# Kernel optimization log

Hardware: AMD Instinct MI355X
Metric: run time of the kernel (lower is better)

Reference implementation:

```python
import jax, jax.numpy as jnp
import numpy as np

IN_F, OUT_F = 64, 32
N = IN_F * OUT_F + OUT_F  # 2080 sampled parameters (weights + bias)
B, S = 8, 2048
SCALE_INIT = 1.0 * float(np.sqrt(2.0 / (IN_F + OUT_F)))


def setup_inputs() -> dict:
    key = jax.random.key(0)
    k_x, k_eps, k_loc, k_cov = jax.random.split(key, 4)
    x = jax.random.normal(k_x, (B, S, IN_F), dtype=jnp.float32)
    eps = jax.random.normal(k_eps, (B, S, N), dtype=jnp.float32)
    loc = 0.01 * jax.random.normal(k_loc, (N,), dtype=jnp.float32)
    logvar = jnp.full((N,), float(np.log(SCALE_INIT)), dtype=jnp.float32)
    n_off = N * (N - 1) // 2
    cov_flat = 0.001 * jax.random.normal(k_cov, (n_off,), dtype=jnp.float32)
    return {"x": x, "eps": eps, "loc": loc, "logvar": logvar, "cov_flat": cov_flat}


def reference(x, eps, loc, logvar, cov_flat):
    n = loc.shape[0]
    in_f = x.shape[-1]
    out_f = n // (in_f + 1)  # n = out*(in+1)
    # flat_to_triangular (strictly lower) + make_cholesky, vectorized scatter
    rows, cols = np.tril_indices(n, -1)
    A = jnp.zeros((n, n), dtype=x.dtype).at[rows, cols].set(cov_flat)
    L = A + jnp.diag(jnp.exp(logvar * 0.5))  # off-diag from cov, diag = std
    # MultivariateNormal rsample: loc + L @ eps (per batch sample)
    W = loc + jnp.einsum('bsn,mn->bsm', eps, L)  # [B,S,N]
    b = W[..., :out_f]
    Wm = W[..., out_f:].reshape(*W.shape[:-1], in_f, out_f)  # [B,S,in,out]
    y = jnp.einsum('bsh,bshk->bsk', x, Wm) + b
    return y
```

## Files before the change

### kernel.cpp

```cpp
#include <hip/hip_runtime.h>
#include <hip/hip_bf16.h>

#define IN_F  64
#define OUT_F 32
#define NV    2080
#define NPAD  2176
#define MM    16384
#define KK    2080
#define NBN   17
#define BM    256

typedef __attribute__((ext_vector_type(4))) float f32x4;
typedef __bf16 bf16x8 __attribute__((ext_vector_type(8)));

using gas_ptr = const __attribute__((address_space(1))) void*;
using lds_ptr = __attribute__((address_space(3))) void*;

__global__ __launch_bounds__(256) void build_L_k(const float* __restrict__ cov,
                                                 const float* __restrict__ logvar,
                                                 __hip_bfloat16* __restrict__ LB) {
    const int idx = blockIdx.x * 256 + threadIdx.x;
    const int m = idx / KK;
    const int k = idx - m * KK;
    float v = 0.0f;
    if (m < NV) {
        if (k < m)       v = cov[(size_t)(m * (m - 1) / 2) + k];
        else if (k == m) v = expf(0.5f * logvar[m]);
    }
    LB[idx] = __float2bfloat16(v);
}

__global__ __launch_bounds__(256, 2) void gemm_v6_k(const float* __restrict__ A,
                                                    const __hip_bfloat16* __restrict__ BT,
                                                    const float* __restrict__ loc,
                                                    const float* __restrict__ x,
                                                    float* __restrict__ Ypart) {
    __shared__ __align__(16) __hip_bfloat16 Bs[3][128 * 32];
    __shared__ float xs[BM][4];

    const int tid  = threadIdx.x;
    const int bm   = blockIdx.x;
    const int bn   = (NBN - 1) - blockIdx.y;
    const int wave = tid >> 6;
    const int lane = tid & 63;
    const int quad = lane >> 4;
    const int r16  = lane & 15;
    const int kblocks = min(KK / 32, 4 * bn + 4);

    {
        const int row = bm * BM + tid;
#pragma unroll
        for (int c = 0; c < 4; c++) {
            const int h = 4 * bn - 1 + c;
            float w = 0.0f;
            if (bn == 0 && c == 0)       w = 1.0f;
            else if (h >= 0 && h < IN_F) w = x[(size_t)row * IN_F + h];
            xs[tid][c] = w;
        }
    }

    const float*          __restrict__ Ag = A  + (size_t)bm * BM * KK;
    const __hip_bfloat16* __restrict__ Bg = BT + (size_t)bn * 128 * KK;

    size_t arofs[4];
#pragma unroll
    for (int i = 0; i < 4; i++) {
        const int row = 64 * wave + 16 * i + r16;
        arofs[i] = (size_t)row * KK + (size_t)(quad * 8);
    }

    size_t bgofs[2]; int bldso[2];
#pragma unroll
    for (int u = 0; u < 2; u++) {
        const int c = tid + 256 * u;
        const int r = c >> 2, p = (c & 3) ^ ((r >> 1) & 3);
        bgofs[u] = (size_t)r * KK + (size_t)(p * 8);
        bldso[u] = c * 8;
    }

    int bofs[8];
#pragma unroll
    for (int j = 0; j < 8; j++) {
        const int brow = 16 * j + r16;
        bofs[j] = brow * 32 + (quad ^ ((brow >> 1) & 3)) * 8;
    }

    f32x4 acc[4][8];
#pragma unroll
    for (int i = 0; i < 4; i++)
#pragma unroll
        for (int j = 0; j < 8; j++) acc[i][j] = f32x4{0.f, 0.f, 0.f, 0.f};

    f32x4  ra[8];
    bf16x8 af[4];

    auto loadA = [&](int t) __attribute__((always_inline)) {
        const float* p = Ag + (size_t)t * 32;
#pragma unroll
        for (int i = 0; i < 4; i++) {
            ra[2 * i]     = *(const f32x4*)(p + arofs[i]);
            ra[2 * i + 1] = *(const f32x4*)(p + arofs[i] + 4);
        }
    };
    auto cvtA = [&]() __attribute__((always_inline)) {
#pragma unroll
        for (int i = 0; i < 4; i++) {
#pragma unroll
            for (int q = 0; q < 4; q++) {
                af[i][q]     = (__bf16)ra[2 * i][q];
                af[i][4 + q] = (__bf16)ra[2 * i + 1][q];
            }
        }
    };
    auto stageB = [&](int t, int buf) __attribute__((always_inline)) {
        const __hip_bfloat16* bp = Bg + (size_t)t * 32;
#pragma unroll
        for (int u = 0; u < 2; u++)
            __builtin_amdgcn_global_load_lds((gas_ptr)(bp + bgofs[u]),
                                             (lds_ptr)(&Bs[buf][0] + bldso[u]), 16, 0, 0);
    };

    stageB(0, 0);
    loadA(0);
    stageB(1, 1);
    __builtin_amdgcn_sched_barrier(0);
    asm volatile("s_waitcnt vmcnt(2)" ::: "memory");
    cvtA();
    asm volatile("s_waitcnt lgkmcnt(0)" ::: "memory");
    __builtin_amdgcn_s_barrier();
    __builtin_amdgcn_sched_barrier(0);

    auto iter = [&](int t, int jlo) __attribute__((always_inline)) {
        const bool pfA = (t + 1 < kblocks);
        const bool pfB = (t + 2 < kblocks);
        if (pfA) loadA(t + 1);
        if (pfB) stageB(t + 2, (t + 2) % 3);
        __builtin_amdgcn_sched_barrier(0);

        const __hip_bfloat16* bs = &Bs[t % 3][0];
        __builtin_amdgcn_s_setprio(1);
#pragma unroll
        for (int j = 0; j < 8; j++) {
            if (j >= jlo) {
                const bf16x8 bfr = *(const bf16x8*)(bs + bofs[j]);
#pragma unroll
                for (int i = 0; i < 4; i++)
                    acc[i][j] = __builtin_amdgcn_mfma_f32_16x16x32_bf16(af[i], bfr, acc[i][j], 0, 0, 0);
            }
        }
        __builtin_amdgcn_s_setprio(0);

        if (pfA) {
            if (pfB) { asm volatile("s_waitcnt vmcnt(2)" ::: "memory"); }
            else     { asm volatile("s_waitcnt vmcnt(0)" ::: "memory"); }
            cvtA();
            __builtin_amdgcn_s_barrier();
            __builtin_amdgcn_sched_barrier(0);
        }
    };

    const int t_full = min(kblocks, 4 * bn + 1);
    int t = 0;
    for (; t < t_full; ++t) iter(t, 0);
    for (; t < kblocks; ++t)
        iter(t, 2 * t - 8 * bn);

    float locv[8];
#pragma unroll
    for (int j = 0; j < 8; j++) {
        const int col = bn * 128 + 16 * j + r16;
        locv[j] = (col < NV) ? loc[col] : 0.0f;
    }

    float* yp = Ypart + ((size_t)bn * MM + (size_t)bm * BM) * OUT_F;
#pragma unroll
    for (int i = 0; i < 4; i++) {
#pragma unroll
        for (int r = 0; r < 4; r++) {
            const int tl = 64 * wave + 16 * i + 4 * quad + r;
            float v0 = 0.0f, v1 = 0.0f;
#pragma unroll
            for (int c = 0; c < 4; c++) {
                const float w = xs[tl][c];
                v0 += w * (acc[i][2 * c][r]     + locv[2 * c]);
                v1 += w * (acc[i][2 * c + 1][r] + locv[2 * c + 1]);
            }
            yp[(size_t)tl * OUT_F + r16]      = v0;
            yp[(size_t)tl * OUT_F + 16 + r16] = v1;
        }
    }
}

__global__ __launch_bounds__(256) void reduce_y_k(const float4* __restrict__ yp,
                                                  float4* __restrict__ y) {
    const size_t i = (size_t)blockIdx.x * 256 + threadIdx.x;
    float4 s = yp[i];
#pragma unroll
    for (int b = 1; b < NBN; b++) {
        float4 v = yp[i + (size_t)b * (MM * OUT_F / 4)];
        s.x += v.x; s.y += v.y; s.z += v.z; s.w += v.w;
    }
    y[i] = s;
}

extern "C" void kernel_launch(void* const* d_in, const int* in_sizes, int n_in,
                              void* d_out, int out_size, void* d_ws, size_t ws_size,
                              hipStream_t stream) {
    const float* x      = (const float*)d_in[0];
    const float* eps    = (const float*)d_in[1];
    const float* loc    = (const float*)d_in[2];
    const float* logvar = (const float*)d_in[3];
    const float* cov    = (const float*)d_in[4];
    float* y = (float*)d_out;

    char* ws = (char*)d_ws;
    const size_t lb_bytes = (size_t)NPAD * KK * 2;
    __hip_bfloat16* LB    = (__hip_bfloat16*)ws;
    float*          Ypart = (float*)(ws + lb_bytes);

    build_L_k<<<(NPAD * KK) / 256, 256, 0, stream>>>(cov, logvar, LB);
    gemm_v6_k<<<dim3(MM / BM, NBN), 256, 0, stream>>>(eps, LB, loc, x, Ypart);
    reduce_y_k<<<(MM * OUT_F / 4) / 256, 256, 0, stream>>>((const float4*)Ypart, (float4*)y);
}
```

Before: 357.0 us.

## Stage fp32 eps through LDS and pre-pack L into MFMA fragment order

```diff
diff --git a/kernel.cpp b/kernel.cpp
--- a/kernel.cpp
+++ b/kernel.cpp
@@ -4,10 +4,10 @@
 #define IN_F  64
 #define OUT_F 32
 #define NV    2080
-#define NPAD  2176
 #define MM    16384
 #define KK    2080
 #define NBN   17
+#define NKT   65
 #define BM    256
 
 typedef __attribute__((ext_vector_type(4))) float f32x4;
@@ -16,26 +16,38 @@
 using gas_ptr = const __attribute__((address_space(1))) void*;
 using lds_ptr = __attribute__((address_space(3))) void*;
 
-__global__ __launch_bounds__(256) void build_L_k(const float* __restrict__ cov,
-                                                 const float* __restrict__ logvar,
-                                                 __hip_bfloat16* __restrict__ LB) {
-    const int idx = blockIdx.x * 256 + threadIdx.x;
-    const int m = idx / KK;
-    const int k = idx - m * KK;
-    float v = 0.0f;
-    if (m < NV) {
-        if (k < m)       v = cov[(size_t)(m * (m - 1) / 2) + k];
-        else if (k == m) v = expf(0.5f * logvar[m]);
-    }
-    LB[idx] = __float2bfloat16(v);
-}
-
-__global__ __launch_bounds__(256, 2) void gemm_v6_k(const float* __restrict__ A,
-                                                    const __hip_bfloat16* __restrict__ BT,
+__global__ __launch_bounds__(256) void build_L2_k(const float* __restrict__ cov,
+                                                  const float* __restrict__ logvar,
+                                                  __hip_bfloat16* __restrict__ LB2) {
+    const int idx  = blockIdx.x * 256 + threadIdx.x;
+    const int lane = idx & 63;
+    const int j    = (idx >> 6) & 7;
+    const int rem  = idx >> 9;
+    const int t    = rem % NKT;
+    const int bn   = rem / NKT;
+    const int row  = bn * 128 + 16 * j + (lane & 15);
+    const int k0   = t * 32 + (lane >> 4) * 8;
+
+    bf16x8 w;
+#pragma unroll
+    for (int e = 0; e < 8; e++) {
+        const int k = k0 + e;
+        float v = 0.0f;
+        if (row < NV) {
+            if (k < row)       v = cov[(size_t)(row * (row - 1) / 2) + k];
+            else if (k == row) v = expf(0.5f * logvar[row]);
+        }
+        w[e] = (__bf16)v;
+    }
+    *(bf16x8*)(LB2 + (size_t)idx * 8) = w;
+}
+
+__global__ __launch_bounds__(256, 2) void gemm_v7_k(const float* __restrict__ A,
+                                                    const __hip_bfloat16* __restrict__ BT2,
                                                     const float* __restrict__ loc,
                                                     const float* __restrict__ x,
                                                     float* __restrict__ Ypart) {
-    __shared__ __align__(16) __hip_bfloat16 Bs[3][128 * 32];
+    __shared__ __align__(16) float As[2][BM * 32];
     __shared__ float xs[BM][4];
 
     const int tid  = threadIdx.x;
@@ -45,7 +57,7 @@
     const int lane = tid & 63;
     const int quad = lane >> 4;
     const int r16  = lane & 15;
-    const int kblocks = min(KK / 32, 4 * bn + 4);
+    const int kblocks = min(NKT, 4 * bn + 4);
 
     {
         const int row = bm * BM + tid;
@@ -59,30 +71,25 @@
         }
     }
 
-    const float*          __restrict__ Ag = A  + (size_t)bm * BM * KK;
-    const __hip_bfloat16* __restrict__ Bg = BT + (size_t)bn * 128 * KK;
-
-    size_t arofs[4];
+    const float* __restrict__ Ag = A + (size_t)bm * BM * KK;
+    const __hip_bfloat16* __restrict__ Bg2 =
+        BT2 + (size_t)bn * NKT * 4096;
+
+    size_t sofs[8]; int dofs[8];
+#pragma unroll
+    for (int u = 0; u < 8; u++) {
+        const int c = tid + 256 * u;
+        const int r = c >> 3, o = (c & 7) ^ (r & 7);
+        sofs[u] = (size_t)r * KK + (size_t)(o * 4);
+        dofs[u] = c * 4;
+    }
+
+    int aof0[4], aof1[4];
 #pragma unroll
     for (int i = 0; i < 4; i++) {
         const int row = 64 * wave + 16 * i + r16;
-        arofs[i] = (size_t)row * KK + (size_t)(quad * 8);
-    }
-
-    size_t bgofs[2]; int bldso[2];
-#pragma unroll
-    for (int u = 0; u < 2; u++) {
-        const int c = tid + 256 * u;
-        const int r = c >> 2, p = (c & 3) ^ ((r >> 1) & 3);
-        bgofs[u] = (size_t)r * KK + (size_t)(p * 8);
-        bldso[u] = c * 8;
-    }
-
-    int bofs[8];
-#pragma unroll
-    for (int j = 0; j < 8; j++) {
-        const int brow = 16 * j + r16;
-        bofs[j] = brow * 32 + (quad ^ ((brow >> 1) & 3)) * 8;
+        aof0[i] = (row * 8 + ((2 * quad)     ^ (row & 7))) * 4;
+        aof1[i] = (row * 8 + ((2 * quad + 1) ^ (row & 7))) * 4;
     }
 
     f32x4 acc[4][8];
@@ -91,69 +98,59 @@
 #pragma unroll
         for (int j = 0; j < 8; j++) acc[i][j] = f32x4{0.f, 0.f, 0.f, 0.f};
 
-    f32x4  ra[8];
-    bf16x8 af[4];
-
-    auto loadA = [&](int t) __attribute__((always_inline)) {
+    bf16x8 bcur[8];
+
+    auto stageA = [&](int t, int buf) __attribute__((always_inline)) {
         const float* p = Ag + (size_t)t * 32;
 #pragma unroll
-        for (int i = 0; i < 4; i++) {
-            ra[2 * i]     = *(const f32x4*)(p + arofs[i]);
-            ra[2 * i + 1] = *(const f32x4*)(p + arofs[i] + 4);
-        }
+        for (int u = 0; u < 8; u++)
+            __builtin_amdgcn_global_load_lds((gas_ptr)(p + sofs[u]),
+                                             (lds_ptr)(&As[buf][0] + dofs[u]), 16, 0, 0);
     };
-    auto cvtA = [&]() __attribute__((always_inline)) {
-#pragma unroll
-        for (int i = 0; i < 4; i++) {
-#pragma unroll
-            for (int q = 0; q < 4; q++) {
-                af[i][q]     = (__bf16)ra[2 * i][q];
-                af[i][4 + q] = (__bf16)ra[2 * i + 1][q];
-            }
-        }
+    auto loadB = [&](int t) __attribute__((always_inline)) {
+        const __hip_bfloat16* p = Bg2 + (size_t)t * 4096 + lane * 8;
+#pragma unroll
+        for (int j = 0; j < 8; j++)
+            bcur[j] = *(const bf16x8*)(p + j * 512);
     };
-    auto stageB = [&](int t, int buf) __attribute__((always_inline)) {
-        const __hip_bfloat16* bp = Bg + (size_t)t * 32;
-#pragma unroll
-        for (int u = 0; u < 2; u++)
-            __builtin_amdgcn_global_load_lds((gas_ptr)(bp + bgofs[u]),
-                                             (lds_ptr)(&Bs[buf][0] + bldso[u]), 16, 0, 0);
-    };
-
-    stageB(0, 0);
-    loadA(0);
-    stageB(1, 1);
+
+    stageA(0, 0);
+    loadB(0);
     __builtin_amdgcn_sched_barrier(0);
-    asm volatile("s_waitcnt vmcnt(2)" ::: "memory");
-    cvtA();
+    asm volatile("s_waitcnt vmcnt(8)" ::: "memory");
     asm volatile("s_waitcnt lgkmcnt(0)" ::: "memory");
     __builtin_amdgcn_s_barrier();
     __builtin_amdgcn_sched_barrier(0);
 
     auto iter = [&](int t, int jlo) __attribute__((always_inline)) {
-        const bool pfA = (t + 1 < kblocks);
-        const bool pfB = (t + 2 < kblocks);
-        if (pfA) loadA(t + 1);
-        if (pfB) stageB(t + 2, (t + 2) % 3);
+        const bool pf = (t + 1 < kblocks);
+        if (pf) stageA(t + 1, (t + 1) & 1);
         __builtin_amdgcn_sched_barrier(0);
 
-        const __hip_bfloat16* bs = &Bs[t % 3][0];
-        __builtin_amdgcn_s_setprio(1);
+        const float* as = &As[t & 1][0];
+        bf16x8 af[4];
+#pragma unroll
+        for (int i = 0; i < 4; i++) {
+            const f32x4 x0 = *(const f32x4*)(as + aof0[i]);
+            const f32x4 x1 = *(const f32x4*)(as + aof1[i]);
+#pragma unroll
+            for (int q = 0; q < 4; q++) {
+                af[i][q]     = (__bf16)x0[q];
+                af[i][4 + q] = (__bf16)x1[q];
+            }
+        }
 #pragma unroll
         for (int j = 0; j < 8; j++) {
             if (j >= jlo) {
-                const bf16x8 bfr = *(const bf16x8*)(bs + bofs[j]);
 #pragma unroll
                 for (int i = 0; i < 4; i++)
-                    acc[i][j] = __builtin_amdgcn_mfma_f32_16x16x32_bf16(af[i], bfr, acc[i][j], 0, 0, 0);
+                    acc[i][j] = __builtin_amdgcn_mfma_f32_16x16x32_bf16(af[i], bcur[j], acc[i][j], 0, 0, 0);
             }
         }
-        __builtin_amdgcn_s_setprio(0);
-
-        if (pfA) {
-            if (pfB) { asm volatile("s_waitcnt vmcnt(2)" ::: "memory"); }
-            else     { asm volatile("s_waitcnt vmcnt(0)" ::: "memory"); }
-            cvtA();
+
+        if (pf) {
+            loadB(t + 1);
+            asm volatile("s_waitcnt vmcnt(8)" ::: "memory");
             __builtin_amdgcn_s_barrier();
             __builtin_amdgcn_sched_barrier(0);
         }
@@ -214,11 +211,11 @@
     float* y = (float*)d_out;
 
     char* ws = (char*)d_ws;
-    const size_t lb_bytes = (size_t)NPAD * KK * 2;
-    __hip_bfloat16* LB    = (__hip_bfloat16*)ws;
-    float*          Ypart = (float*)(ws + lb_bytes);
-
-    build_L_k<<<(NPAD * KK) / 256, 256, 0, stream>>>(cov, logvar, LB);
-    gemm_v6_k<<<dim3(MM / BM, NBN), 256, 0, stream>>>(eps, LB, loc, x, Ypart);
+    const size_t lb2_bytes = (size_t)NBN * NKT * 4096 * 2;
+    __hip_bfloat16* LB2   = (__hip_bfloat16*)ws;
+    float*          Ypart = (float*)(ws + lb2_bytes);
+
+    build_L2_k<<<(NBN * NKT * 8 * 64) / 256, 256, 0, stream>>>(cov, logvar, LB2);
+    gemm_v7_k<<<dim3(MM / BM, NBN), 256, 0, stream>>>(eps, LB2, loc, x, Ypart);
     reduce_y_k<<<(MM * OUT_F / 4) / 256, 256, 0, stream>>>((const float4*)Ypart, (float4*)y);
 }
```

Result: faster. 323.1 us (-9.5%).

## Widen GEMM tile to 256 columns and stage fp32 eps through LDS

Applied to the files above, without the earlier changes.

```diff
diff --git a/kernel.cpp b/kernel.cpp
--- a/kernel.cpp
+++ b/kernel.cpp
@@ -4,10 +4,12 @@
 #define IN_F  64
 #define OUT_F 32
 #define NV    2080
-#define NPAD  2176
+#define NPAD2 2304
 #define MM    16384
 #define KK    2080
 #define NBN   17
+#define NP    9
+#define NKT   65
 #define BM    256
 
 typedef __attribute__((ext_vector_type(4))) float f32x4;
@@ -30,58 +32,72 @@
     LB[idx] = __float2bfloat16(v);
 }
 
-__global__ __launch_bounds__(256, 2) void gemm_v6_k(const float* __restrict__ A,
+__global__ __launch_bounds__(512, 2) void gemm_v8_k(const float* __restrict__ A,
                                                     const __hip_bfloat16* __restrict__ BT,
                                                     const float* __restrict__ loc,
                                                     const float* __restrict__ x,
                                                     float* __restrict__ Ypart) {
-    __shared__ __align__(16) __hip_bfloat16 Bs[3][128 * 32];
-    __shared__ float xs[BM][4];
+    __shared__ __align__(16) float          As[3][BM * 32];
+    __shared__ __align__(16) __hip_bfloat16 Bs[3][BM * 32];
+    __shared__ float xs[BM][8];
 
     const int tid  = threadIdx.x;
     const int bm   = blockIdx.x;
-    const int bn   = (NBN - 1) - blockIdx.y;
+    const int p    = (NP - 1) - blockIdx.y;
     const int wave = tid >> 6;
     const int lane = tid & 63;
     const int quad = lane >> 4;
     const int r16  = lane & 15;
-    const int kblocks = min(KK / 32, 4 * bn + 4);
+    const int wr   = wave >> 1;
+    const int wc   = wave & 1;
+    const int bnw  = 2 * p + wc;
+    const bool act = (bnw < NBN);
+    const int kmax = (p < 8) ? (8 * p + 8) : NKT;
 
     {
-        const int row = bm * BM + tid;
+        const int rw = tid >> 1, pr = tid & 1;
+        const int row = bm * BM + rw;
 #pragma unroll
         for (int c = 0; c < 4; c++) {
-            const int h = 4 * bn - 1 + c;
+            const int h = 8 * p + 4 * pr - 1 + c;
             float w = 0.0f;
-            if (bn == 0 && c == 0)       w = 1.0f;
-            else if (h >= 0 && h < IN_F) w = x[(size_t)row * IN_F + h];
-            xs[tid][c] = w;
+            if (p == 0 && pr == 0 && c == 0)  w = 1.0f;
+            else if (h >= 0 && h < IN_F)      w = x[(size_t)row * IN_F + h];
+            xs[rw][4 * pr + c] = w;
         }
     }
 
     const float*          __restrict__ Ag = A  + (size_t)bm * BM * KK;
-    const __hip_bfloat16* __restrict__ Bg = BT + (size_t)bn * 128 * KK;
-
-    size_t arofs[4];
+    const __hip_bfloat16* __restrict__ Bg = BT + (size_t)(BM * p) * KK;
+
+    size_t agofs[4]; int aldso[4];
+#pragma unroll
+    for (int u = 0; u < 4; u++) {
+        const int c = tid + 512 * u;
+        const int r = c >> 3, o = (c & 7) ^ (r & 7);
+        agofs[u] = (size_t)r * KK + (size_t)(o * 4);
+        aldso[u] = c * 4;
+    }
+    size_t bgofs[2]; int bldso[2];
+#pragma unroll
+    for (int u = 0; u < 2; u++) {
+        const int c = tid + 512 * u;
+        const int r = c >> 2, pp = (c & 3) ^ ((r >> 1) & 3);
+        bgofs[u] = (size_t)r * KK + (size_t)(pp * 8);
+        bldso[u] = c * 8;
+    }
+
+    int aof0[4], aof1[4];
 #pragma unroll
     for (int i = 0; i < 4; i++) {
-        const int row = 64 * wave + 16 * i + r16;
-        arofs[i] = (size_t)row * KK + (size_t)(quad * 8);
-    }
-
-    size_t bgofs[2]; int bldso[2];
-#pragma unroll
-    for (int u = 0; u < 2; u++) {
-        const int c = tid + 256 * u;
-        const int r = c >> 2, p = (c & 3) ^ ((r >> 1) & 3);
-        bgofs[u] = (size_t)r * KK + (size_t)(p * 8);
-        bldso[u] = c * 8;
-    }
-
+        const int row = 64 * wr + 16 * i + r16;
+        aof0[i] = (row * 8 + ((2 * quad)     ^ (row & 7))) * 4;
+        aof1[i] = (row * 8 + ((2 * quad + 1) ^ (row & 7))) * 4;
+    }
     int bofs[8];
 #pragma unroll
     for (int j = 0; j < 8; j++) {
-        const int brow = 16 * j + r16;
+        const int brow = 128 * wc + 16 * j + r16;
         bofs[j] = brow * 32 + (quad ^ ((brow >> 1) & 3)) * 8;
     }
 
@@ -91,28 +107,12 @@
 #pragma unroll
         for (int j = 0; j < 8; j++) acc[i][j] = f32x4{0.f, 0.f, 0.f, 0.f};
 
-    f32x4  ra[8];
-    bf16x8 af[4];
-
-    auto loadA = [&](int t) __attribute__((always_inline)) {
-        const float* p = Ag + (size_t)t * 32;
-#pragma unroll
-        for (int i = 0; i < 4; i++) {
-            ra[2 * i]     = *(const f32x4*)(p + arofs[i]);
-            ra[2 * i + 1] = *(const f32x4*)(p + arofs[i] + 4);
-        }
-    };
-    auto cvtA = [&]() __attribute__((always_inline)) {
-#pragma unroll
-        for (int i = 0; i < 4; i++) {
-#pragma unroll
-            for (int q = 0; q < 4; q++) {
-                af[i][q]     = (__bf16)ra[2 * i][q];
-                af[i][4 + q] = (__bf16)ra[2 * i + 1][q];
-            }
-        }
-    };
-    auto stageB = [&](int t, int buf) __attribute__((always_inline)) {
+    auto stage = [&](int t, int buf) __attribute__((always_inline)) {
+        const float* ap = Ag + (size_t)t * 32;
+#pragma unroll
+        for (int u = 0; u < 4; u++)
+            __builtin_amdgcn_global_load_lds((gas_ptr)(ap + agofs[u]),
+                                             (lds_ptr)(&As[buf][0] + aldso[u]), 16, 0, 0);
         const __hip_bfloat16* bp = Bg + (size_t)t * 32;
 #pragma unroll
         for (int u = 0; u < 2; u++)
@@ -120,73 +120,86 @@
                                              (lds_ptr)(&Bs[buf][0] + bldso[u]), 16, 0, 0);
     };
 
-    stageB(0, 0);
-    loadA(0);
-    stageB(1, 1);
+    stage(0, 0);
+    stage(1, 1);
     __builtin_amdgcn_sched_barrier(0);
-    asm volatile("s_waitcnt vmcnt(2)" ::: "memory");
-    cvtA();
+    asm volatile("s_waitcnt vmcnt(6)" ::: "memory");
     asm volatile("s_waitcnt lgkmcnt(0)" ::: "memory");
     __builtin_amdgcn_s_barrier();
     __builtin_amdgcn_sched_barrier(0);
 
     auto iter = [&](int t, int jlo) __attribute__((always_inline)) {
-        const bool pfA = (t + 1 < kblocks);
-        const bool pfB = (t + 2 < kblocks);
-        if (pfA) loadA(t + 1);
-        if (pfB) stageB(t + 2, (t + 2) % 3);
+        const bool pf2 = (t + 2 < kmax);
+        if (pf2) stage(t + 2, (t + 2) % 3);
         __builtin_amdgcn_sched_barrier(0);
 
-        const __hip_bfloat16* bs = &Bs[t % 3][0];
-        __builtin_amdgcn_s_setprio(1);
-#pragma unroll
-        for (int j = 0; j < 8; j++) {
-            if (j >= jlo) {
-                const bf16x8 bfr = *(const bf16x8*)(bs + bofs[j]);
-#pragma unroll
-                for (int i = 0; i < 4; i++)
-                    acc[i][j] = __builtin_amdgcn_mfma_f32_16x16x32_bf16(af[i], bfr, acc[i][j], 0, 0, 0);
+        if (act && jlo < 8) {
+            const float*          as = &As[t % 3][0];
+            const __hip_bfloat16* bs = &Bs[t % 3][0];
+            bf16x8 af[4];
+#pragma unroll
+            for (int i = 0; i < 4; i++) {
+                const f32x4 x0 = *(const f32x4*)(as + aof0[i]);
+                const f32x4 x1 = *(const f32x4*)(as + aof1[i]);
+#pragma unroll
+                for (int q = 0; q < 4; q++) {
+                    af[i][q]     = (__bf16)x0[q];
+                    af[i][4 + q] = (__bf16)x1[q];
+                }
             }
-        }
-        __builtin_amdgcn_s_setprio(0);
-
-        if (pfA) {
-            if (pfB) { asm volatile("s_waitcnt vmcnt(2)" ::: "memory"); }
+            __builtin_amdgcn_s_setprio(1);
+#pragma unroll
+            for (int j = 0; j < 8; j++) {
+                if (j >= jlo) {
+                    const bf16x8 bfr = *(const bf16x8*)(bs + bofs[j]);
+#pragma unroll
+                    for (int i = 0; i < 4; i++)
+                        acc[i][j] = __builtin_amdgcn_mfma_f32_16x16x32_bf16(af[i], bfr, acc[i][j], 0, 0, 0);
+                }
+            }
+            __builtin_amdgcn_s_setprio(0);
+        }
+
+        if (t + 1 < kmax) {
+            if (pf2) { asm volatile("s_waitcnt vmcnt(6)" ::: "memory"); }
             else     { asm volatile("s_waitcnt vmcnt(0)" ::: "memory"); }
-            cvtA();
             __builtin_amdgcn_s_barrier();
             __builtin_amdgcn_sched_barrier(0);
         }
     };
 
-    const int t_full = min(kblocks, 4 * bn + 1);
+    const int t_full = min(kmax, 8 * p + 1);
     int t = 0;
     for (; t < t_full; ++t) iter(t, 0);
-    for (; t < kblocks; ++t)
-        iter(t, 2 * t - 8 * bn);
-
-    float locv[8];
-#pragma unroll
-    for (int j = 0; j < 8; j++) {
-        const int col = bn * 128 + 16 * j + r16;
-        locv[j] = (col < NV) ? loc[col] : 0.0f;
-    }
-
-    float* yp = Ypart + ((size_t)bn * MM + (size_t)bm * BM) * OUT_F;
-#pragma unroll
-    for (int i = 0; i < 4; i++) {
-#pragma unroll
-        for (int r = 0; r < 4; r++) {
-            const int tl = 64 * wave + 16 * i + 4 * quad + r;
-            float v0 = 0.0f, v1 = 0.0f;
-#pragma unroll
-            for (int c = 0; c < 4; c++) {
-                const float w = xs[tl][c];
-                v0 += w * (acc[i][2 * c][r]     + locv[2 * c]);
-                v1 += w * (acc[i][2 * c + 1][r] + locv[2 * c + 1]);
+    for (; t < kmax; ++t) {
+        int jl = 2 * t - 8 * bnw;
+        jl = jl < 0 ? 0 : (jl > 8 ? 8 : jl);
+        iter(t, jl);
+    }
+
+    if (act) {
+        float locv[8];
+#pragma unroll
+        for (int j = 0; j < 8; j++) {
+            const int col = bnw * 128 + 16 * j + r16;
+            locv[j] = (col < NV) ? loc[col] : 0.0f;
+        }
+        float* yp = Ypart + ((size_t)bnw * MM + (size_t)bm * BM) * OUT_F;
+#pragma unroll
+        for (int i = 0; i < 4; i++) {
+#pragma unroll
+            for (int r = 0; r < 4; r++) {
+                const int tl = 64 * wr + 16 * i + 4 * quad + r;
+                float v0 = 0.0f, v1 = 0.0f;
+#pragma unroll
+                for (int c = 0; c < 4; c++) {
+                    const float w = xs[tl][4 * wc + c];
+                    v0 += w * (acc[i][2 * c][r]     + locv[2 * c]);
+                    v1 += w * (acc[i][2 * c + 1][r] + locv[2 * c + 1]);
+                }
+                yp[(size_t)tl * OUT_F + r16]      = v0;
+                yp[(size_t)tl * OUT_F + 16 + r16] = v1;
             }
-            yp[(size_t)tl * OUT_F + r16]      = v0;
-            yp[(size_t)tl * OUT_F + 16 + r16] = v1;
         }
     }
 }
@@ -214,11 +227,11 @@
     float* y = (float*)d_out;
 
     char* ws = (char*)d_ws;
-    const size_t lb_bytes = (size_t)NPAD * KK * 2;
+    const size_t lb_bytes = (size_t)NPAD2 * KK * 2;
     __hip_bfloat16* LB    = (__hip_bfloat16*)ws;
     float*          Ypart = (float*)(ws + lb_bytes);
 
-    build_L_k<<<(NPAD * KK) / 256, 256, 0, stream>>>(cov, logvar, LB);
-    gemm_v6_k<<<dim3(MM / BM, NBN), 256, 0, stream>>>(eps, LB, loc, x, Ypart);
+    build_L_k<<<(NPAD2 * KK) / 256, 256, 0, stream>>>(cov, logvar, LB);
+    gemm_v8_k<<<dim3(MM / BM, NP), 512, 0, stream>>>(eps, LB, loc, x, Ypart);
     reduce_y_k<<<(MM * OUT_F / 4) / 256, 256, 0, stream>>>((const float4*)Ypart, (float4*)y);
 }
```

After: 356.3 us. About the same (-0.2%).
